# Performance work log

Hardware: AMD Instinct MI355X
Metric: run time of the kernel (lower is better)

The kernel has to match this reference:

```python
import jax, jax.numpy as jnp
import numpy as np

B, S, D, H, DK, DV = 2, 2048, 1024, 16, 64, 64


def setup_inputs() -> dict:
    key = jax.random.key(0)
    ks = jax.random.split(key, 12)
    s = 0.02
    return {
        "q": jax.random.normal(ks[0], (B, S, D), jnp.float32),
        "k": jax.random.normal(ks[1], (B, S, D), jnp.float32),
        "v": jax.random.normal(ks[2], (B, S, D), jnp.float32),
        "attn_mask": jax.random.bernoulli(ks[3], 0.1, (B, S, S)),
        "wq": jax.random.normal(ks[4], (D, H * DK), jnp.float32) * s,
        "bq": jnp.zeros((H * DK,), jnp.float32),
        "wk": jax.random.normal(ks[5], (D, H * DK), jnp.float32) * s,
        "bk": jnp.zeros((H * DK,), jnp.float32),
        "wv": jax.random.normal(ks[6], (D, H * DV), jnp.float32) * s,
        "bv": jnp.zeros((H * DV,), jnp.float32),
        "wo": jax.random.normal(ks[7], (H * DV, D), jnp.float32) * s,
        "bo": jnp.zeros((D,), jnp.float32),
        "gamma": jnp.ones((D,), jnp.float32),
        "beta": jnp.zeros((D,), jnp.float32),
    }


def reference(q, k, v, attn_mask, wq, bq, wk, bk, wv, bv, wo, bo, gamma, beta):
    residual = q
    # projections -> [B, H, S, dk/dv]
    qh = (q @ wq + bq).reshape(B, S, H, DK).transpose(0, 2, 1, 3)
    kh = (k @ wk + bk).reshape(B, S, H, DK).transpose(0, 2, 1, 3)
    vh = (v @ wv + bv).reshape(B, S, H, DV).transpose(0, 2, 1, 3)
    scores = jnp.einsum("bhqd,bhkd->bhqk", qh, kh) / np.sqrt(DK).astype(np.float32)
    scores = jnp.where(attn_mask[:, None, :, :], jnp.float32(-1e9), scores)
    attn = jax.nn.softmax(scores, axis=-1)
    context = jnp.einsum("bhqk,bhkd->bhqd", attn, vh)
    context = context.transpose(0, 2, 1, 3).reshape(B, S, H * DV)
    out = context @ wo + bo + residual
    # LayerNorm (eps=1e-5, torch default)
    mu = out.mean(-1, keepdims=True)
    var = out.var(-1, keepdims=True)
    out = (out - mu) * jax.lax.rsqrt(var + 1e-5) * gamma + beta
    return out, attn
```

## Files before the change

### kernel.cpp

```cpp
#include <hip/hip_runtime.h>
#include <hip/hip_bf16.h>

#define BB 2
#define SS 2048
#define DD 1024
#define HH 16
#define DKV 64

typedef __attribute__((ext_vector_type(8))) short short8;
typedef __attribute__((ext_vector_type(4))) short short4_t;
typedef __attribute__((ext_vector_type(4))) float f32x4;

#define MFMA16(a, b, c) __builtin_amdgcn_mfma_f32_16x16x32_bf16(a, b, c, 0, 0, 0)

__device__ __forceinline__ short f2bf(float f) {
    __hip_bfloat16 h = __float2bfloat16(f);
    union { __hip_bfloat16 h; short s; } u;
    u.h = h;
    return u.s;
}

__global__ __launch_bounds__(256) void wtrans_kernel(
    const float* __restrict__ w0, const float* __restrict__ w1,
    const float* __restrict__ w2, const float* __restrict__ w3,
    const float* __restrict__ qf, const float* __restrict__ kf, const float* __restrict__ vf,
    short* __restrict__ o0, short* __restrict__ o1,
    short* __restrict__ o2, short* __restrict__ o3,
    short* __restrict__ oq, short* __restrict__ ok, short* __restrict__ ov)
{
    const int z = blockIdx.z;
    const int t = threadIdx.x;
    if (z >= 4) {
        const float* src = (z == 4) ? qf : (z == 5) ? kf : vf;
        short* dst = (z == 4) ? oq : (z == 5) ? ok : ov;
        size_t idx = ((size_t)(blockIdx.y * 16 + blockIdx.x) * 256 + t) * 8;
        #pragma unroll
        for (int it = 0; it < 8; ++it, idx += 524288) {
            float4 a = *(const float4*)(src + idx);
            float4 b = *(const float4*)(src + idx + 4);
            short8 p = { f2bf(a.x), f2bf(a.y), f2bf(a.z), f2bf(a.w),
                         f2bf(b.x), f2bf(b.y), f2bf(b.z), f2bf(b.w) };
            *(short8*)(dst + idx) = p;
        }
        return;
    }
    const float* W = (z == 0) ? w0 : (z == 1) ? w1 : (z == 2) ? w2 : w3;
    short* O = (z == 0) ? o0 : (z == 1) ? o1 : (z == 2) ? o2 : o3;
    __shared__ short T[64][72];
    const int k0 = blockIdx.x * 64, n0 = blockIdx.y * 64;
    const int row = t >> 2, c = (t & 3) * 16;
    const float* src = W + (size_t)(k0 + row) * DD + n0 + c;
    #pragma unroll
    for (int i = 0; i < 16; i += 4) {
        float4 f = *(const float4*)(src + i);
        T[c + i + 0][row] = f2bf(f.x);
        T[c + i + 1][row] = f2bf(f.y);
        T[c + i + 2][row] = f2bf(f.z);
        T[c + i + 3][row] = f2bf(f.w);
    }
    __syncthreads();
    const int nr = t >> 2, kc = (t & 3) * 16;
    *(short8*)(O + (size_t)(n0 + nr) * DD + k0 + kc)     = *(const short8*)&T[nr][kc];
    *(short8*)(O + (size_t)(n0 + nr) * DD + k0 + kc + 8) = *(const short8*)&T[nr][kc + 8];
}

__global__ __launch_bounds__(256) void proj3_kernel(
    const short* __restrict__ A0, const short* __restrict__ A1, const short* __restrict__ A2,
    const short* __restrict__ WT0, const short* __restrict__ WT1, const short* __restrict__ WT2,
    const float* __restrict__ bq, const float* __restrict__ bk, const float* __restrict__ bv,
    __hip_bfloat16* __restrict__ o0, __hip_bfloat16* __restrict__ o1, __hip_bfloat16* __restrict__ o2,
    const int* __restrict__ mask, unsigned long long* __restrict__ bits)
{
    const int t = threadIdx.x;
    const int lane = t & 63;
    const int wave = t >> 6;

    if (blockIdx.z == 0) {
        const int bid = blockIdx.y * 32 + blockIdx.x;
        const int base = bid * 512 + wave * 128;
        #pragma unroll 4
        for (int wi = base; wi < base + 128; ++wi) {
            const int mv = mask[(size_t)wi * 64 + lane];
            const unsigned long long bal = __ballot(mv != 0);
            if (lane == 0) bits[wi] = bal;
        }
        return;
    }

    const int z = blockIdx.z - 1;
    const short* A  = (z == 0) ? A0 : (z == 1) ? A1 : A2;
    const short* WT = (z == 0) ? WT0 : (z == 1) ? WT1 : WT2;
    const float* bias = (z == 0) ? bq : (z == 1) ? bk : bv;
    __hip_bfloat16* outh = (z == 0) ? o0 : (z == 1) ? o1 : o2;

    __shared__ __align__(16) short As[128][40];
    __shared__ __align__(16) short Bs[128][40];
    const int wm = wave >> 1, wn = wave & 1;
    const int m0 = blockIdx.x * 128, n0 = blockIdx.y * 128;
    const int lr = lane & 15;
    const int kb = (lane >> 4) * 8;
    const int row2 = t >> 1, kk2 = (t & 1) * 16;

    f32x4 acc[4][4] = {};

    for (int k0 = 0; k0 < DD; k0 += 32) {
        __syncthreads();
        {
            const short8* srca = (const short8*)(A + (size_t)(m0 + row2) * DD + k0 + kk2);
            *(short8*)&As[row2][kk2]     = srca[0];
            *(short8*)&As[row2][kk2 + 8] = srca[1];
        }
        {
            const short8* srcw = (const short8*)(WT + (size_t)(n0 + row2) * DD + k0 + kk2);
            *(short8*)&Bs[row2][kk2]     = srcw[0];
            *(short8*)&Bs[row2][kk2 + 8] = srcw[1];
        }
        __syncthreads();
        short8 af[4], bfr[4];
        #pragma unroll
        for (int i = 0; i < 4; i++) af[i]  = *(const short8*)&As[wm * 64 + i * 16 + lr][kb];
        #pragma unroll
        for (int j = 0; j < 4; j++) bfr[j] = *(const short8*)&Bs[wn * 64 + j * 16 + lr][kb];
        #pragma unroll
        for (int i = 0; i < 4; i++)
            #pragma unroll
            for (int j = 0; j < 4; j++)
                acc[i][j] = MFMA16(af[i], bfr[j], acc[i][j]);
    }

    if (z != 2) {
        #pragma unroll
        for (int j = 0; j < 4; j++) {
            const int col = n0 + wn * 64 + j * 16 + lr;
            const float bvv = bias[col];
            const int h = col >> 6, d = col & 63;
            #pragma unroll
            for (int i = 0; i < 4; i++) {
                #pragma unroll
                for (int r = 0; r < 4; r++) {
                    const int m = m0 + wm * 64 + i * 16 + (lane >> 4) * 4 + r;
                    const int b = m >> 11, s = m & (SS - 1);
                    outh[(((size_t)(b * HH + h)) * SS + s) * DKV + d] =
                        __float2bfloat16(acc[i][j][r] + bvv);
                }
            }
        }
    } else {
        short* vT = (short*)outh;
        #pragma unroll
        for (int j = 0; j < 4; j++) {
            const int col = n0 + wn * 64 + j * 16 + lr;
            const float bvv = bias[col];
            const int h = col >> 6, d = col & 63;
            #pragma unroll
            for (int i = 0; i < 4; i++) {
                const int m = m0 + wm * 64 + i * 16 + (lane >> 4) * 4;
                const int b = m >> 11, s = m & (SS - 1);
                short4_t pk;
                #pragma unroll
                for (int r = 0; r < 4; r++) pk[r] = f2bf(acc[i][j][r] + bvv);
                *(short4_t*)(vT + ((size_t)(b * HH + h) * DKV + d) * SS + s) = pk;
            }
        }
    }
}

__global__ __launch_bounds__(512) void attn_compute_kernel(
    const __hip_bfloat16* __restrict__ qh, const __hip_bfloat16* __restrict__ kh,
    const __hip_bfloat16* __restrict__ vT, const unsigned long long* __restrict__ bits,
    float* __restrict__ linvb, __hip_bfloat16* __restrict__ ctx)
{
    __shared__ __align__(16) short Ks[2][64][72];
    __shared__ __align__(16) short Vs[2][64][72];
    __shared__ __align__(16) short Ps[8][16][72];
    const int t = threadIdx.x, lane = t & 63, w = t >> 6;

    const int logical = (blockIdx.x & 7) * 64 + (blockIdx.x >> 3);
    const int qt = logical & 15;
    const int bh = logical >> 4;
    const int h = bh & (HH - 1);
    const int b = bh >> 4;
    const int q0w = qt * 128 + w * 16;
    const size_t headbase = (size_t)bh * SS * DKV;
    const int lr = lane & 15;
    const int kb = (lane >> 4) * 8;
    const int Q4 = lane >> 4;
    const int rbase = Q4 * 4;

    const short* kbase = (const short*)kh + headbase;
    const short* vbase = (const short*)vT + (size_t)bh * DKV * SS;
    const unsigned long long* bitrow = bits + ((size_t)b * SS + q0w) * (SS / 64);

    const int srow = t >> 3, sc8 = (t & 7) * 8;
    const short* kstg = kbase + (size_t)srow * DKV + sc8;
    const short* vstg = vbase + (size_t)srow * SS + sc8;

    const short* qrp = (const short*)qh + headbase + (size_t)(q0w + lr) * DKV;
    const short8 aq0 = *(const short8*)(qrp + kb);
    const short8 aq1 = *(const short8*)(qrp + 32 + kb);

    float lsum[4] = {0.f, 0.f, 0.f, 0.f};
    f32x4 cacc[4] = {};

    {
        short8 kreg = *(const short8*)(kstg);
        short8 vreg = *(const short8*)(vstg);
        *(short8*)&Ks[0][srow][sc8] = kreg;
        *(short8*)&Vs[0][srow][sc8] = vreg;
        __syncthreads();
        for (int kt = 0; kt < 32; ++kt) {
            const int cur = kt & 1;
            if (kt + 1 < 32) {
                kreg = *(const short8*)(kstg + (size_t)(kt + 1) * 64 * DKV);
                vreg = *(const short8*)(vstg + (size_t)(kt + 1) * 64);
            }
            f32x4 sc[4];
            __builtin_amdgcn_s_setprio(1);
            #pragma unroll
            for (int fc = 0; fc < 4; ++fc) {
                short8 bk0 = *(const short8*)&Ks[cur][fc * 16 + lr][kb];
                short8 bk1 = *(const short8*)&Ks[cur][fc * 16 + lr][32 + kb];
                f32x4 s = {0.f, 0.f, 0.f, 0.f};
                s = MFMA16(aq0, bk0, s);
                s = MFMA16(aq1, bk1, s);
                sc[fc] = s;
            }
            __builtin_amdgcn_s_setprio(0);
            unsigned long long mw[4];
            #pragma unroll
            for (int r = 0; r < 4; ++r)
                mw[r] = bitrow[(size_t)(rbase + r) * (SS / 64) + kt];
            #pragma unroll
            for (int fc = 0; fc < 4; ++fc)
                #pragma unroll
                for (int r = 0; r < 4; ++r) {
                    const bool masked = (mw[r] >> (fc * 16 + lr)) & 1ull;
                    const float p = masked ? 0.f : __expf(sc[fc][r] * 0.125f);
                    lsum[r] += p;
                    Ps[w][rbase + r][fc * 16 + lr] = f2bf(p);
                }
            short8 ap0 = *(const short8*)&Ps[w][lr][kb];
            short8 ap1 = *(const short8*)&Ps[w][lr][32 + kb];
            __builtin_amdgcn_s_setprio(1);
            #pragma unroll
            for (int fd = 0; fd < 4; ++fd) {
                short8 bv0 = *(const short8*)&Vs[cur][fd * 16 + lr][kb];
                short8 bv1 = *(const short8*)&Vs[cur][fd * 16 + lr][32 + kb];
                cacc[fd] = MFMA16(ap0, bv0, cacc[fd]);
                cacc[fd] = MFMA16(ap1, bv1, cacc[fd]);
            }
            __builtin_amdgcn_s_setprio(0);
            if (kt + 1 < 32) {
                *(short8*)&Ks[cur ^ 1][srow][sc8] = kreg;
                *(short8*)&Vs[cur ^ 1][srow][sc8] = vreg;
            }
            __syncthreads();
        }
    }
    #pragma unroll
    for (int r = 0; r < 4; r++) {
        float s = lsum[r];
        s += __shfl_xor(s, 1);
        s += __shfl_xor(s, 2);
        s += __shfl_xor(s, 4);
        s += __shfl_xor(s, 8);
        lsum[r] = s;
    }
    float linv[4];
    #pragma unroll
    for (int r = 0; r < 4; r++) linv[r] = 1.f / lsum[r];

    if (lr == 0) {
        #pragma unroll
        for (int r = 0; r < 4; r++)
            linvb[(size_t)bh * SS + q0w + rbase + r] = linv[r];
    }

    #pragma unroll
    for (int fd = 0; fd < 4; ++fd)
        #pragma unroll
        for (int r = 0; r < 4; r++) {
            const int qrow = q0w + rbase + r;
            ctx[((size_t)b * SS + qrow) * DD + h * DKV + fd * 16 + lr] =
                __float2bfloat16(cacc[fd][r] * linv[r]);
        }
}

__global__ __launch_bounds__(256) void outstore_kernel(
    const __hip_bfloat16* __restrict__ Actx, const short* __restrict__ WT,
    const float* __restrict__ bias, const float* __restrict__ resid,
    float* __restrict__ out,
    const __hip_bfloat16* __restrict__ qh, const __hip_bfloat16* __restrict__ kh,
    const unsigned long long* __restrict__ bits, const float* __restrict__ linvb,
    float* __restrict__ attn)
{
    __shared__ __align__(16) short LDSBUF[36864];
    const int t = threadIdx.x, lane = t & 63, w = t >> 6;
    const int lr = lane & 15;
    const int kb = (lane >> 4) * 8;

    if (blockIdx.z == 0) {
        short (*As)[40] = (short(*)[40])LDSBUF;
        short (*Bs)[40] = (short(*)[40])(LDSBUF + 5120);
        const int wave = w;
        const int wm = wave >> 1, wn = wave & 1;
        const int m0 = blockIdx.x * 128, n0 = blockIdx.y * 128;
        const int row2 = t >> 1, kk2 = (t & 1) * 16;

        f32x4 acc[4][4] = {};

        for (int k0 = 0; k0 < DD; k0 += 32) {
            __syncthreads();
            {
                const short8* src = (const short8*)((const short*)Actx + (size_t)(m0 + row2) * DD + k0 + kk2);
                *(short8*)&As[row2][kk2]     = src[0];
                *(short8*)&As[row2][kk2 + 8] = src[1];
            }
            {
                const short8* srcw = (const short8*)(WT + (size_t)(n0 + row2) * DD + k0 + kk2);
                *(short8*)&Bs[row2][kk2]     = srcw[0];
                *(short8*)&Bs[row2][kk2 + 8] = srcw[1];
            }
            __syncthreads();
            short8 af[4], bfr[4];
            #pragma unroll
            for (int i = 0; i < 4; i++) af[i]  = *(const short8*)&As[wm * 64 + i * 16 + lr][kb];
            #pragma unroll
            for (int j = 0; j < 4; j++) bfr[j] = *(const short8*)&Bs[wn * 64 + j * 16 + lr][kb];
            #pragma unroll
            for (int i = 0; i < 4; i++)
                #pragma unroll
                for (int j = 0; j < 4; j++)
                    acc[i][j] = MFMA16(af[i], bfr[j], acc[i][j]);
        }

        #pragma unroll
        for (int j = 0; j < 4; j++) {
            const int col = n0 + wn * 64 + j * 16 + lr;
            const float bvv = bias[col];
            #pragma unroll
            for (int i = 0; i < 4; i++) {
                #pragma unroll
                for (int r = 0; r < 4; r++) {
                    const int m = m0 + wm * 64 + i * 16 + (lane >> 4) * 4 + r;
                    out[(size_t)m * DD + col] = acc[i][j][r] + bvv + resid[(size_t)m * DD + col];
                }
            }
        }
        return;
    }

    short (*Ks)[72] = (short(*)[72])LDSBUF;
    const int sb = (blockIdx.z - 1) * 256 + blockIdx.y * 32 + blockIdx.x;
    const int qt = sb & 31;
    const int kc = (sb >> 5) & 3;
    const int bh = sb >> 7;
    const int b = bh >> 4;
    const int q0w = qt * 64 + w * 16;
    const int k0c = kc * 512;
    const size_t headbase = (size_t)bh * SS * DKV;
    const int Q4 = lane >> 4;
    const int rbase = Q4 * 4;

    {
        const short* kbase = (const short*)kh + headbase + (size_t)k0c * DKV;
        const int c8 = (t & 7) * 8;
        #pragma unroll
        for (int sweep = 0; sweep < 16; ++sweep) {
            const int row = (t >> 3) + sweep * 32;
            *(short8*)&Ks[row][c8] = *(const short8*)(kbase + (size_t)row * DKV + c8);
        }
    }

    const short* qrp = (const short*)qh + headbase + (size_t)(q0w + lr) * DKV;
    const short8 aq0 = *(const short8*)(qrp + kb);
    const short8 aq1 = *(const short8*)(qrp + 32 + kb);

    float linv[4];
    #pragma unroll
    for (int r = 0; r < 4; ++r)
        linv[r] = linvb[(size_t)bh * SS + q0w + rbase + r];

    const unsigned long long* bitrow = bits + ((size_t)b * SS + q0w) * (SS / 64);
    float* arow = attn + ((size_t)bh * SS + q0w) * SS + k0c;

    __syncthreads();

    for (int g = 0; g < 8; ++g) {
        unsigned long long mw[4];
        #pragma unroll
        for (int r = 0; r < 4; ++r)
            mw[r] = bitrow[(size_t)(rbase + r) * (SS / 64) + kc * 8 + g];
        #pragma unroll
        for (int fc = 0; fc < 4; ++fc) {
            const int col = g * 64 + fc * 16;
            short8 bk0 = *(const short8*)&Ks[col + lr][kb];
            short8 bk1 = *(const short8*)&Ks[col + lr][32 + kb];
            f32x4 s = {0.f, 0.f, 0.f, 0.f};
            s = MFMA16(aq0, bk0, s);
            s = MFMA16(aq1, bk1, s);
            #pragma unroll
            for (int r = 0; r < 4; ++r) {
                const bool masked = (mw[r] >> (fc * 16 + lr)) & 1ull;
                const float p = masked ? 0.f : __expf(s[r] * 0.125f) * linv[r];
                arow[(size_t)(rbase + r) * SS + col + lr] = p;
            }
        }
    }
}

__global__ __launch_bounds__(256) void ln_kernel(
    float* __restrict__ io, const float* __restrict__ g, const float* __restrict__ bta)
{
    const int row = blockIdx.x;
    const int t = threadIdx.x;
    float* p = io + (size_t)row * DD;
    float4 x = *(float4*)(p + t * 4);
    float s  = x.x + x.y + x.z + x.w;
    float s2 = x.x * x.x + x.y * x.y + x.z * x.z + x.w * x.w;
    #pragma unroll
    for (int off = 32; off; off >>= 1) {
        s  += __shfl_xor(s, off);
        s2 += __shfl_xor(s2, off);
    }
    __shared__ float as_[4], bs_[4];
    const int w = t >> 6, l = t & 63;
    if (!l) { as_[w] = s; bs_[w] = s2; }
    __syncthreads();
    s  = as_[0] + as_[1] + as_[2] + as_[3];
    s2 = bs_[0] + bs_[1] + bs_[2] + bs_[3];
    const float mu  = s * (1.f / DD);
    const float var = s2 * (1.f / DD) - mu * mu;
    const float rs  = rsqrtf(var + 1e-5f);
    float4 gv = *(const float4*)(g + t * 4);
    float4 bv = *(const float4*)(bta + t * 4);
    float4 o;
    o.x = (x.x - mu) * rs * gv.x + bv.x;
    o.y = (x.y - mu) * rs * gv.y + bv.y;
    o.z = (x.z - mu) * rs * gv.z + bv.z;
    o.w = (x.w - mu) * rs * gv.w + bv.w;
    *(float4*)(p + t * 4) = o;
}

extern "C" void kernel_launch(void* const* d_in, const int* in_sizes, int n_in,
                              void* d_out, int out_size, void* d_ws, size_t ws_size,
                              hipStream_t stream)
{
    (void)in_sizes; (void)n_in; (void)out_size; (void)ws_size;
    const float* q     = (const float*)d_in[0];
    const float* k     = (const float*)d_in[1];
    const float* v     = (const float*)d_in[2];
    const int*   mask  = (const int*)d_in[3];
    const float* wq    = (const float*)d_in[4];
    const float* bq    = (const float*)d_in[5];
    const float* wk    = (const float*)d_in[6];
    const float* bk    = (const float*)d_in[7];
    const float* wv    = (const float*)d_in[8];
    const float* bv    = (const float*)d_in[9];
    const float* wo    = (const float*)d_in[10];
    const float* bo    = (const float*)d_in[11];
    const float* gamma = (const float*)d_in[12];
    const float* beta  = (const float*)d_in[13];

    float* out  = (float*)d_out;
    float* attn = out + (size_t)BB * SS * DD;

    const size_t hsz = (size_t)BB * HH * SS * DKV;
    __hip_bfloat16* qhp = (__hip_bfloat16*)d_ws;
    __hip_bfloat16* khp = qhp + hsz;
    __hip_bfloat16* vTp = khp + hsz;
    __hip_bfloat16* ctx = vTp + hsz;
    unsigned long long* bits = (unsigned long long*)(ctx + hsz);
    float* linvb = (float*)(bits + (size_t)BB * SS * (SS / 64));
    short* wtq = (short*)(linvb + (size_t)BB * HH * SS);
    short* wtk = wtq + (size_t)DD * DD;
    short* wtv = wtk + (size_t)DD * DD;
    short* wto = wtv + (size_t)DD * DD;
    short* qb  = wto + (size_t)DD * DD;
    short* kb2 = qb  + (size_t)BB * SS * DD;
    short* vb2 = kb2 + (size_t)BB * SS * DD;

    dim3 gw(16, 16, 7);
    wtrans_kernel<<<gw, 256, 0, stream>>>(wq, wk, wv, wo, q, k, v,
                                          wtq, wtk, wtv, wto, qb, kb2, vb2);

    dim3 gg(32, 8, 4);
    proj3_kernel<<<gg, 256, 0, stream>>>(qb, kb2, vb2, wtq, wtk, wtv, bq, bk, bv,
                                         qhp, khp, vTp, mask, bits);
    attn_compute_kernel<<<BB * HH * 16, 512, 0, stream>>>(qhp, khp, vTp, bits, linvb, ctx);

    dim3 gm(32, 8, 17);
    outstore_kernel<<<gm, 256, 0, stream>>>(ctx, wto, bo, q, out,
                                            qhp, khp, bits, linvb, attn);
    ln_kernel<<<BB * SS, 256, 0, stream>>>(out, gamma, beta);
}
```

Before: 330.3 us.

## Split pipeline per batch into uber-kernels overlapping attention with projections and stores

Restructures the launch sequence so each stage runs per batch. Batch-1 projections and mask packing now share a launch with batch-0 attention, and batch-1 attention shares one with batch-0 output projection and attn store. Attention blocks shrink to 256 threads covering 64 query rows, with wider K/V staging per thread. The goal is to fill idle CUs during low-occupancy phases and hide kernel boundaries. In exchange, the uber-kernels have larger unified LDS footprints that may limit occupancy, and block scheduling order decides how much overlap actually happens.

```diff
diff --git a/kernel.cpp b/kernel.cpp
--- a/kernel.cpp
+++ b/kernel.cpp
@@ -20,97 +20,41 @@
     return u.s;
 }
 
-__global__ __launch_bounds__(256) void wtrans_kernel(
-    const float* __restrict__ w0, const float* __restrict__ w1,
-    const float* __restrict__ w2, const float* __restrict__ w3,
-    const float* __restrict__ qf, const float* __restrict__ kf, const float* __restrict__ vf,
-    short* __restrict__ o0, short* __restrict__ o1,
-    short* __restrict__ o2, short* __restrict__ o3,
-    short* __restrict__ oq, short* __restrict__ ok, short* __restrict__ ov)
-{
-    const int z = blockIdx.z;
-    const int t = threadIdx.x;
-    if (z >= 4) {
-        const float* src = (z == 4) ? qf : (z == 5) ? kf : vf;
-        short* dst = (z == 4) ? oq : (z == 5) ? ok : ov;
-        size_t idx = ((size_t)(blockIdx.y * 16 + blockIdx.x) * 256 + t) * 8;
-        #pragma unroll
-        for (int it = 0; it < 8; ++it, idx += 524288) {
-            float4 a = *(const float4*)(src + idx);
-            float4 b = *(const float4*)(src + idx + 4);
-            short8 p = { f2bf(a.x), f2bf(a.y), f2bf(a.z), f2bf(a.w),
-                         f2bf(b.x), f2bf(b.y), f2bf(b.z), f2bf(b.w) };
-            *(short8*)(dst + idx) = p;
-        }
-        return;
-    }
-    const float* W = (z == 0) ? w0 : (z == 1) ? w1 : (z == 2) ? w2 : w3;
-    short* O = (z == 0) ? o0 : (z == 1) ? o1 : (z == 2) ? o2 : o3;
-    __shared__ short T[64][72];
-    const int k0 = blockIdx.x * 64, n0 = blockIdx.y * 64;
-    const int row = t >> 2, c = (t & 3) * 16;
-    const float* src = W + (size_t)(k0 + row) * DD + n0 + c;
-    #pragma unroll
-    for (int i = 0; i < 16; i += 4) {
-        float4 f = *(const float4*)(src + i);
-        T[c + i + 0][row] = f2bf(f.x);
-        T[c + i + 1][row] = f2bf(f.y);
-        T[c + i + 2][row] = f2bf(f.z);
-        T[c + i + 3][row] = f2bf(f.w);
-    }
-    __syncthreads();
-    const int nr = t >> 2, kc = (t & 3) * 16;
-    *(short8*)(O + (size_t)(n0 + nr) * DD + k0 + kc)     = *(const short8*)&T[nr][kc];
-    *(short8*)(O + (size_t)(n0 + nr) * DD + k0 + kc + 8) = *(const short8*)&T[nr][kc + 8];
-}
-
-__global__ __launch_bounds__(256) void proj3_kernel(
-    const short* __restrict__ A0, const short* __restrict__ A1, const short* __restrict__ A2,
-    const short* __restrict__ WT0, const short* __restrict__ WT1, const short* __restrict__ WT2,
-    const float* __restrict__ bq, const float* __restrict__ bk, const float* __restrict__ bv,
-    __hip_bfloat16* __restrict__ o0, __hip_bfloat16* __restrict__ o1, __hip_bfloat16* __restrict__ o2,
-    const int* __restrict__ mask, unsigned long long* __restrict__ bits)
-{
-    const int t = threadIdx.x;
-    const int lane = t & 63;
-    const int wave = t >> 6;
-
-    if (blockIdx.z == 0) {
-        const int bid = blockIdx.y * 32 + blockIdx.x;
-        const int base = bid * 512 + wave * 128;
-        #pragma unroll 4
-        for (int wi = base; wi < base + 128; ++wi) {
-            const int mv = mask[(size_t)wi * 64 + lane];
-            const unsigned long long bal = __ballot(mv != 0);
-            if (lane == 0) bits[wi] = bal;
-        }
-        return;
-    }
-
-    const int z = blockIdx.z - 1;
-    const short* A  = (z == 0) ? A0 : (z == 1) ? A1 : A2;
-    const short* WT = (z == 0) ? WT0 : (z == 1) ? WT1 : WT2;
-    const float* bias = (z == 0) ? bq : (z == 1) ? bk : bv;
-    __hip_bfloat16* outh = (z == 0) ? o0 : (z == 1) ? o1 : o2;
-
-    __shared__ __align__(16) short As[128][40];
-    __shared__ __align__(16) short Bs[128][40];
+
+__device__ __forceinline__ void body_maskpack(
+    const int* __restrict__ mask, unsigned long long* __restrict__ bits,
+    int batch, int bid128)
+{
+    const int t = threadIdx.x, lane = t & 63, wave = t >> 6;
+    const int base = batch * 65536 + bid128 * 512 + wave * 128;
+    #pragma unroll 4
+    for (int wi = base; wi < base + 128; ++wi) {
+        const int mv = mask[(size_t)wi * 64 + lane];
+        const unsigned long long bal = __ballot(mv != 0);
+        if (lane == 0) bits[wi] = bal;
+    }
+}
+
+__device__ __forceinline__ void body_projgemm(
+    const short* __restrict__ A, const short* __restrict__ WT,
+    const float* __restrict__ bias, short* __restrict__ outp,
+    int zmode, int batch, int bx, int by, short* lds)
+{
+    short (*As)[40] = (short(*)[40])lds;
+    short (*Bs)[40] = (short(*)[40])(lds + 5120);
+    const int t = threadIdx.x, lane = t & 63, wave = t >> 6;
     const int wm = wave >> 1, wn = wave & 1;
-    const int m0 = blockIdx.x * 128, n0 = blockIdx.y * 128;
-    const int lr = lane & 15;
-    const int kb = (lane >> 4) * 8;
+    const int m0 = batch * SS + bx * 128, n0 = by * 128;
+    const int lr = lane & 15, kb = (lane >> 4) * 8;
     const int row2 = t >> 1, kk2 = (t & 1) * 16;
 
     f32x4 acc[4][4] = {};
-
     for (int k0 = 0; k0 < DD; k0 += 32) {
         __syncthreads();
         {
             const short8* srca = (const short8*)(A + (size_t)(m0 + row2) * DD + k0 + kk2);
             *(short8*)&As[row2][kk2]     = srca[0];
             *(short8*)&As[row2][kk2 + 8] = srca[1];
-        }
-        {
             const short8* srcw = (const short8*)(WT + (size_t)(n0 + row2) * DD + k0 + kk2);
             *(short8*)&Bs[row2][kk2]     = srcw[0];
             *(short8*)&Bs[row2][kk2 + 8] = srcw[1];
@@ -128,7 +72,7 @@
                 acc[i][j] = MFMA16(af[i], bfr[j], acc[i][j]);
     }
 
-    if (z != 2) {
+    if (zmode != 2) {
         #pragma unroll
         for (int j = 0; j < 4; j++) {
             const int col = n0 + wn * 64 + j * 16 + lr;
@@ -140,13 +84,12 @@
                 for (int r = 0; r < 4; r++) {
                     const int m = m0 + wm * 64 + i * 16 + (lane >> 4) * 4 + r;
                     const int b = m >> 11, s = m & (SS - 1);
-                    outh[(((size_t)(b * HH + h)) * SS + s) * DKV + d] =
-                        __float2bfloat16(acc[i][j][r] + bvv);
+                    outp[(((size_t)(b * HH + h)) * SS + s) * DKV + d] =
+                        f2bf(acc[i][j][r] + bvv);
                 }
             }
         }
     } else {
-        short* vT = (short*)outh;
         #pragma unroll
         for (int j = 0; j < 4; j++) {
             const int col = n0 + wn * 64 + j * 16 + lr;
@@ -159,103 +102,107 @@
                 short4_t pk;
                 #pragma unroll
                 for (int r = 0; r < 4; r++) pk[r] = f2bf(acc[i][j][r] + bvv);
-                *(short4_t*)(vT + ((size_t)(b * HH + h) * DKV + d) * SS + s) = pk;
+                *(short4_t*)(outp + ((size_t)(b * HH + h) * DKV + d) * SS + s) = pk;
             }
         }
     }
 }
 
-__global__ __launch_bounds__(512) void attn_compute_kernel(
-    const __hip_bfloat16* __restrict__ qh, const __hip_bfloat16* __restrict__ kh,
-    const __hip_bfloat16* __restrict__ vT, const unsigned long long* __restrict__ bits,
-    float* __restrict__ linvb, __hip_bfloat16* __restrict__ ctx)
-{
-    __shared__ __align__(16) short Ks[2][64][72];
-    __shared__ __align__(16) short Vs[2][64][72];
-    __shared__ __align__(16) short Ps[8][16][72];
+__device__ __forceinline__ void body_attn(
+    const short* __restrict__ qh, const short* __restrict__ kh,
+    const short* __restrict__ vT, const unsigned long long* __restrict__ bits,
+    float* __restrict__ linvb, short* __restrict__ ctx,
+    int batch, int logical, short* lds)
+{
+    short (*Ks)[64][72] = (short(*)[64][72])lds;
+    short (*Vs)[64][72] = (short(*)[64][72])(lds + 9216);
+    short (*Ps)[16][72] = (short(*)[16][72])(lds + 18432);
     const int t = threadIdx.x, lane = t & 63, w = t >> 6;
-
-    const int logical = (blockIdx.x & 7) * 64 + (blockIdx.x >> 3);
-    const int qt = logical & 15;
-    const int bh = logical >> 4;
-    const int h = bh & (HH - 1);
-    const int b = bh >> 4;
-    const int q0w = qt * 128 + w * 16;
+    const int qt = logical & 31;
+    const int h  = logical >> 5;
+    const int bh = batch * HH + h;
+    const int q0w = qt * 64 + w * 16;
     const size_t headbase = (size_t)bh * SS * DKV;
-    const int lr = lane & 15;
-    const int kb = (lane >> 4) * 8;
-    const int Q4 = lane >> 4;
-    const int rbase = Q4 * 4;
-
-    const short* kbase = (const short*)kh + headbase;
-    const short* vbase = (const short*)vT + (size_t)bh * DKV * SS;
-    const unsigned long long* bitrow = bits + ((size_t)b * SS + q0w) * (SS / 64);
-
-    const int srow = t >> 3, sc8 = (t & 7) * 8;
+    const int lr = lane & 15, kb = (lane >> 4) * 8;
+    const int rbase = (lane >> 4) * 4;
+
+    const short* kbase = kh + headbase;
+    const short* vbase = vT + (size_t)bh * DKV * SS;
+    const unsigned long long* bitrow = bits + ((size_t)batch * SS + q0w) * (SS / 64);
+
+    const int srow = t >> 2, sc8 = (t & 3) * 16;
     const short* kstg = kbase + (size_t)srow * DKV + sc8;
     const short* vstg = vbase + (size_t)srow * SS + sc8;
 
-    const short* qrp = (const short*)qh + headbase + (size_t)(q0w + lr) * DKV;
+    const short* qrp = qh + headbase + (size_t)(q0w + lr) * DKV;
     const short8 aq0 = *(const short8*)(qrp + kb);
     const short8 aq1 = *(const short8*)(qrp + 32 + kb);
 
     float lsum[4] = {0.f, 0.f, 0.f, 0.f};
     f32x4 cacc[4] = {};
 
-    {
-        short8 kreg = *(const short8*)(kstg);
-        short8 vreg = *(const short8*)(vstg);
-        *(short8*)&Ks[0][srow][sc8] = kreg;
-        *(short8*)&Vs[0][srow][sc8] = vreg;
+    short8 ka = *(const short8*)(kstg);
+    short8 kc = *(const short8*)(kstg + 8);
+    short8 va = *(const short8*)(vstg);
+    short8 vc = *(const short8*)(vstg + 8);
+    *(short8*)&Ks[0][srow][sc8]     = ka;
+    *(short8*)&Ks[0][srow][sc8 + 8] = kc;
+    *(short8*)&Vs[0][srow][sc8]     = va;
+    *(short8*)&Vs[0][srow][sc8 + 8] = vc;
+    __syncthreads();
+    for (int kt = 0; kt < 32; ++kt) {
+        const int cur = kt & 1;
+        if (kt + 1 < 32) {
+            const short* kn = kstg + (size_t)(kt + 1) * 64 * DKV;
+            const short* vn = vstg + (size_t)(kt + 1) * 64;
+            ka = *(const short8*)(kn);
+            kc = *(const short8*)(kn + 8);
+            va = *(const short8*)(vn);
+            vc = *(const short8*)(vn + 8);
+        }
+        f32x4 sc[4];
+        __builtin_amdgcn_s_setprio(1);
+        #pragma unroll
+        for (int fc = 0; fc < 4; ++fc) {
+            short8 bk0 = *(const short8*)&Ks[cur][fc * 16 + lr][kb];
+            short8 bk1 = *(const short8*)&Ks[cur][fc * 16 + lr][32 + kb];
+            f32x4 s = {0.f, 0.f, 0.f, 0.f};
+            s = MFMA16(aq0, bk0, s);
+            s = MFMA16(aq1, bk1, s);
+            sc[fc] = s;
+        }
+        __builtin_amdgcn_s_setprio(0);
+        unsigned long long mw[4];
+        #pragma unroll
+        for (int r = 0; r < 4; ++r)
+            mw[r] = bitrow[(size_t)(rbase + r) * (SS / 64) + kt];
+        #pragma unroll
+        for (int fc = 0; fc < 4; ++fc)
+            #pragma unroll
+            for (int r = 0; r < 4; ++r) {
+                const bool masked = (mw[r] >> (fc * 16 + lr)) & 1ull;
+                const float p = masked ? 0.f : __expf(sc[fc][r] * 0.125f);
+                lsum[r] += p;
+                Ps[w][rbase + r][fc * 16 + lr] = f2bf(p);
+            }
+        short8 ap0 = *(const short8*)&Ps[w][lr][kb];
+        short8 ap1 = *(const short8*)&Ps[w][lr][32 + kb];
+        __builtin_amdgcn_s_setprio(1);
+        #pragma unroll
+        for (int fd = 0; fd < 4; ++fd) {
+            short8 bv0 = *(const short8*)&Vs[cur][fd * 16 + lr][kb];
+            short8 bv1 = *(const short8*)&Vs[cur][fd * 16 + lr][32 + kb];
+            cacc[fd] = MFMA16(ap0, bv0, cacc[fd]);
+            cacc[fd] = MFMA16(ap1, bv1, cacc[fd]);
+        }
+        __builtin_amdgcn_s_setprio(0);
+        if (kt + 1 < 32) {
+            *(short8*)&Ks[cur ^ 1][srow][sc8]     = ka;
+            *(short8*)&Ks[cur ^ 1][srow][sc8 + 8] = kc;
+            *(short8*)&Vs[cur ^ 1][srow][sc8]     = va;
+            *(short8*)&Vs[cur ^ 1][srow][sc8 + 8] = vc;
+        }
         __syncthreads();
-        for (int kt = 0; kt < 32; ++kt) {
-            const int cur = kt & 1;
-            if (kt + 1 < 32) {
-                kreg = *(const short8*)(kstg + (size_t)(kt + 1) * 64 * DKV);
-                vreg = *(const short8*)(vstg + (size_t)(kt + 1) * 64);
-            }
-            f32x4 sc[4];
-            __builtin_amdgcn_s_setprio(1);
-            #pragma unroll
-            for (int fc = 0; fc < 4; ++fc) {
-                short8 bk0 = *(const short8*)&Ks[cur][fc * 16 + lr][kb];
-                short8 bk1 = *(const short8*)&Ks[cur][fc * 16 + lr][32 + kb];
-                f32x4 s = {0.f, 0.f, 0.f, 0.f};
-                s = MFMA16(aq0, bk0, s);
-                s = MFMA16(aq1, bk1, s);
-                sc[fc] = s;
-            }
-            __builtin_amdgcn_s_setprio(0);
-            unsigned long long mw[4];
-            #pragma unroll
-            for (int r = 0; r < 4; ++r)
-                mw[r] = bitrow[(size_t)(rbase + r) * (SS / 64) + kt];
-            #pragma unroll
-            for (int fc = 0; fc < 4; ++fc)
-                #pragma unroll
-                for (int r = 0; r < 4; ++r) {
-                    const bool masked = (mw[r] >> (fc * 16 + lr)) & 1ull;
-                    const float p = masked ? 0.f : __expf(sc[fc][r] * 0.125f);
-                    lsum[r] += p;
-                    Ps[w][rbase + r][fc * 16 + lr] = f2bf(p);
-                }
-            short8 ap0 = *(const short8*)&Ps[w][lr][kb];
-            short8 ap1 = *(const short8*)&Ps[w][lr][32 + kb];
-            __builtin_amdgcn_s_setprio(1);
-            #pragma unroll
-            for (int fd = 0; fd < 4; ++fd) {
-                short8 bv0 = *(const short8*)&Vs[cur][fd * 16 + lr][kb];
-                short8 bv1 = *(const short8*)&Vs[cur][fd * 16 + lr][32 + kb];
-                cacc[fd] = MFMA16(ap0, bv0, cacc[fd]);
-                cacc[fd] = MFMA16(ap1, bv1, cacc[fd]);
-            }
-            __builtin_amdgcn_s_setprio(0);
-            if (kt + 1 < 32) {
-                *(short8*)&Ks[cur ^ 1][srow][sc8] = kreg;
-                *(short8*)&Vs[cur ^ 1][srow][sc8] = vreg;
-            }
-            __syncthreads();
-        }
     }
     #pragma unroll
     for (int r = 0; r < 4; r++) {
@@ -275,104 +222,95 @@
         for (int r = 0; r < 4; r++)
             linvb[(size_t)bh * SS + q0w + rbase + r] = linv[r];
     }
-
     #pragma unroll
     for (int fd = 0; fd < 4; ++fd)
         #pragma unroll
         for (int r = 0; r < 4; r++) {
             const int qrow = q0w + rbase + r;
-            ctx[((size_t)b * SS + qrow) * DD + h * DKV + fd * 16 + lr] =
-                __float2bfloat16(cacc[fd][r] * linv[r]);
-        }
-}
-
-__global__ __launch_bounds__(256) void outstore_kernel(
-    const __hip_bfloat16* __restrict__ Actx, const short* __restrict__ WT,
+            ctx[((size_t)batch * SS + qrow) * DD + h * DKV + fd * 16 + lr] =
+                f2bf(cacc[fd][r] * linv[r]);
+        }
+}
+
+__device__ __forceinline__ void body_outproj(
+    const short* __restrict__ Actx, const short* __restrict__ WT,
     const float* __restrict__ bias, const float* __restrict__ resid,
-    float* __restrict__ out,
-    const __hip_bfloat16* __restrict__ qh, const __hip_bfloat16* __restrict__ kh,
+    float* __restrict__ out, int batch, int bx, int by, short* lds)
+{
+    short (*As)[40] = (short(*)[40])lds;
+    short (*Bs)[40] = (short(*)[40])(lds + 5120);
+    const int t = threadIdx.x, lane = t & 63, wave = t >> 6;
+    const int wm = wave >> 1, wn = wave & 1;
+    const int m0 = batch * SS + bx * 128, n0 = by * 128;
+    const int lr = lane & 15, kb = (lane >> 4) * 8;
+    const int row2 = t >> 1, kk2 = (t & 1) * 16;
+
+    f32x4 acc[4][4] = {};
+    for (int k0 = 0; k0 < DD; k0 += 32) {
+        __syncthreads();
+        {
+            const short8* srca = (const short8*)(Actx + (size_t)(m0 + row2) * DD + k0 + kk2);
+            *(short8*)&As[row2][kk2]     = srca[0];
+            *(short8*)&As[row2][kk2 + 8] = srca[1];
+            const short8* srcw = (const short8*)(WT + (size_t)(n0 + row2) * DD + k0 + kk2);
+            *(short8*)&Bs[row2][kk2]     = srcw[0];
+            *(short8*)&Bs[row2][kk2 + 8] = srcw[1];
+        }
+        __syncthreads();
+        short8 af[4], bfr[4];
+        #pragma unroll
+        for (int i = 0; i < 4; i++) af[i]  = *(const short8*)&As[wm * 64 + i * 16 + lr][kb];
+        #pragma unroll
+        for (int j = 0; j < 4; j++) bfr[j] = *(const short8*)&Bs[wn * 64 + j * 16 + lr][kb];
+        #pragma unroll
+        for (int i = 0; i < 4; i++)
+            #pragma unroll
+            for (int j = 0; j < 4; j++)
+                acc[i][j] = MFMA16(af[i], bfr[j], acc[i][j]);
+    }
+    #pragma unroll
+    for (int j = 0; j < 4; j++) {
+        const int col = n0 + wn * 64 + j * 16 + lr;
+        const float bvv = bias[col];
+        #pragma unroll
+        for (int i = 0; i < 4; i++) {
+            #pragma unroll
+            for (int r = 0; r < 4; r++) {
+                const int m = m0 + wm * 64 + i * 16 + (lane >> 4) * 4 + r;
+                out[(size_t)m * DD + col] = acc[i][j][r] + bvv + resid[(size_t)m * DD + col];
+            }
+        }
+    }
+}
+
+__device__ __forceinline__ void body_store(
+    const short* __restrict__ qh, const short* __restrict__ kh,
     const unsigned long long* __restrict__ bits, const float* __restrict__ linvb,
-    float* __restrict__ attn)
-{
-    __shared__ __align__(16) short LDSBUF[36864];
+    float* __restrict__ attn, int batch, int sb, short* lds)
+{
+    short (*Ks)[72] = (short(*)[72])lds;
     const int t = threadIdx.x, lane = t & 63, w = t >> 6;
-    const int lr = lane & 15;
-    const int kb = (lane >> 4) * 8;
-
-    if (blockIdx.z == 0) {
-        short (*As)[40] = (short(*)[40])LDSBUF;
-        short (*Bs)[40] = (short(*)[40])(LDSBUF + 5120);
-        const int wave = w;
-        const int wm = wave >> 1, wn = wave & 1;
-        const int m0 = blockIdx.x * 128, n0 = blockIdx.y * 128;
-        const int row2 = t >> 1, kk2 = (t & 1) * 16;
-
-        f32x4 acc[4][4] = {};
-
-        for (int k0 = 0; k0 < DD; k0 += 32) {
-            __syncthreads();
-            {
-                const short8* src = (const short8*)((const short*)Actx + (size_t)(m0 + row2) * DD + k0 + kk2);
-                *(short8*)&As[row2][kk2]     = src[0];
-                *(short8*)&As[row2][kk2 + 8] = src[1];
-            }
-            {
-                const short8* srcw = (const short8*)(WT + (size_t)(n0 + row2) * DD + k0 + kk2);
-                *(short8*)&Bs[row2][kk2]     = srcw[0];
-                *(short8*)&Bs[row2][kk2 + 8] = srcw[1];
-            }
-            __syncthreads();
-            short8 af[4], bfr[4];
-            #pragma unroll
-            for (int i = 0; i < 4; i++) af[i]  = *(const short8*)&As[wm * 64 + i * 16 + lr][kb];
-            #pragma unroll
-            for (int j = 0; j < 4; j++) bfr[j] = *(const short8*)&Bs[wn * 64 + j * 16 + lr][kb];
-            #pragma unroll
-            for (int i = 0; i < 4; i++)
-                #pragma unroll
-                for (int j = 0; j < 4; j++)
-                    acc[i][j] = MFMA16(af[i], bfr[j], acc[i][j]);
-        }
-
-        #pragma unroll
-        for (int j = 0; j < 4; j++) {
-            const int col = n0 + wn * 64 + j * 16 + lr;
-            const float bvv = bias[col];
-            #pragma unroll
-            for (int i = 0; i < 4; i++) {
-                #pragma unroll
-                for (int r = 0; r < 4; r++) {
-                    const int m = m0 + wm * 64 + i * 16 + (lane >> 4) * 4 + r;
-                    out[(size_t)m * DD + col] = acc[i][j][r] + bvv + resid[(size_t)m * DD + col];
-                }
-            }
-        }
-        return;
-    }
-
-    short (*Ks)[72] = (short(*)[72])LDSBUF;
-    const int sb = (blockIdx.z - 1) * 256 + blockIdx.y * 32 + blockIdx.x;
     const int qt = sb & 31;
     const int kc = (sb >> 5) & 3;
-    const int bh = sb >> 7;
-    const int b = bh >> 4;
+    const int hh = sb >> 7;
+    const int bh = batch * HH + hh;
     const int q0w = qt * 64 + w * 16;
     const int k0c = kc * 512;
     const size_t headbase = (size_t)bh * SS * DKV;
-    const int Q4 = lane >> 4;
-    const int rbase = Q4 * 4;
+    const int lr = lane & 15, kb = (lane >> 4) * 8;
+    const int rbase = (lane >> 4) * 4;
 
     {
-        const short* kbase = (const short*)kh + headbase + (size_t)k0c * DKV;
+        const short* kb2 = kh + headbase + (size_t)k0c * DKV;
         const int c8 = (t & 7) * 8;
         #pragma unroll
         for (int sweep = 0; sweep < 16; ++sweep) {
             const int row = (t >> 3) + sweep * 32;
-            *(short8*)&Ks[row][c8] = *(const short8*)(kbase + (size_t)row * DKV + c8);
-        }
-    }
-
-    const short* qrp = (const short*)qh + headbase + (size_t)(q0w + lr) * DKV;
+            *(short8*)&Ks[row][c8] = *(const short8*)(kb2 + (size_t)row * DKV + c8);
+        }
+    }
+
+    const short* qrp = qh + headbase + (size_t)(q0w + lr) * DKV;
     const short8 aq0 = *(const short8*)(qrp + kb);
     const short8 aq1 = *(const short8*)(qrp + 32 + kb);
 
@@ -381,7 +319,7 @@
     for (int r = 0; r < 4; ++r)
         linv[r] = linvb[(size_t)bh * SS + q0w + rbase + r];
 
-    const unsigned long long* bitrow = bits + ((size_t)b * SS + q0w) * (SS / 64);
+    const unsigned long long* bitrow = bits + ((size_t)batch * SS + q0w) * (SS / 64);
     float* arow = attn + ((size_t)bh * SS + q0w) * SS + k0c;
 
     __syncthreads();
@@ -409,10 +347,10 @@
     }
 }
 
-__global__ __launch_bounds__(256) void ln_kernel(
-    float* __restrict__ io, const float* __restrict__ g, const float* __restrict__ bta)
-{
-    const int row = blockIdx.x;
+__device__ __forceinline__ void body_ln(
+    float* __restrict__ io, const float* __restrict__ g, const float* __restrict__ bta,
+    int row, float* sh)
+{
     const int t = threadIdx.x;
     float* p = io + (size_t)row * DD;
     float4 x = *(float4*)(p + t * 4);
@@ -423,12 +361,11 @@
         s  += __shfl_xor(s, off);
         s2 += __shfl_xor(s2, off);
     }
-    __shared__ float as_[4], bs_[4];
     const int w = t >> 6, l = t & 63;
-    if (!l) { as_[w] = s; bs_[w] = s2; }
+    if (!l) { sh[w] = s; sh[4 + w] = s2; }
     __syncthreads();
-    s  = as_[0] + as_[1] + as_[2] + as_[3];
-    s2 = bs_[0] + bs_[1] + bs_[2] + bs_[3];
+    s  = sh[0] + sh[1] + sh[2] + sh[3];
+    s2 = sh[4] + sh[5] + sh[6] + sh[7];
     const float mu  = s * (1.f / DD);
     const float var = s2 * (1.f / DD) - mu * mu;
     const float rs  = rsqrtf(var + 1e-5f);
@@ -440,6 +377,150 @@
     o.z = (x.z - mu) * rs * gv.z + bv.z;
     o.w = (x.w - mu) * rs * gv.w + bv.w;
     *(float4*)(p + t * 4) = o;
+}
+
+
+__global__ __launch_bounds__(256) void wtrans_kernel(
+    const float* __restrict__ w0, const float* __restrict__ w1,
+    const float* __restrict__ w2, const float* __restrict__ w3,
+    const float* __restrict__ qf, const float* __restrict__ kf, const float* __restrict__ vf,
+    short* __restrict__ o0, short* __restrict__ o1,
+    short* __restrict__ o2, short* __restrict__ o3,
+    short* __restrict__ oq, short* __restrict__ ok, short* __restrict__ ov)
+{
+    const int z = blockIdx.z;
+    const int t = threadIdx.x;
+    if (z >= 4) {
+        const float* src = (z == 4) ? qf : (z == 5) ? kf : vf;
+        short* dst = (z == 4) ? oq : (z == 5) ? ok : ov;
+        size_t idx = ((size_t)(blockIdx.y * 16 + blockIdx.x) * 256 + t) * 8;
+        #pragma unroll
+        for (int it = 0; it < 8; ++it, idx += 524288) {
+            float4 a = *(const float4*)(src + idx);
+            float4 b = *(const float4*)(src + idx + 4);
+            short8 p = { f2bf(a.x), f2bf(a.y), f2bf(a.z), f2bf(a.w),
+                         f2bf(b.x), f2bf(b.y), f2bf(b.z), f2bf(b.w) };
+            *(short8*)(dst + idx) = p;
+        }
+        return;
+    }
+    const float* W = (z == 0) ? w0 : (z == 1) ? w1 : (z == 2) ? w2 : w3;
+    short* O = (z == 0) ? o0 : (z == 1) ? o1 : (z == 2) ? o2 : o3;
+    __shared__ short T[64][72];
+    const int k0 = blockIdx.x * 64, n0 = blockIdx.y * 64;
+    const int row = t >> 2, c = (t & 3) * 16;
+    const float* src = W + (size_t)(k0 + row) * DD + n0 + c;
+    #pragma unroll
+    for (int i = 0; i < 16; i += 4) {
+        float4 f = *(const float4*)(src + i);
+        T[c + i + 0][row] = f2bf(f.x);
+        T[c + i + 1][row] = f2bf(f.y);
+        T[c + i + 2][row] = f2bf(f.z);
+        T[c + i + 3][row] = f2bf(f.w);
+    }
+    __syncthreads();
+    const int nr = t >> 2, kc = (t & 3) * 16;
+    *(short8*)(O + (size_t)(n0 + nr) * DD + k0 + kc)     = *(const short8*)&T[nr][kc];
+    *(short8*)(O + (size_t)(n0 + nr) * DD + k0 + kc + 8) = *(const short8*)&T[nr][kc + 8];
+}
+
+__global__ __launch_bounds__(256) void proj3b_kernel(
+    const short* __restrict__ A0, const short* __restrict__ A1, const short* __restrict__ A2,
+    const short* __restrict__ WT0, const short* __restrict__ WT1, const short* __restrict__ WT2,
+    const float* __restrict__ bq, const float* __restrict__ bk, const float* __restrict__ bv,
+    short* __restrict__ o0, short* __restrict__ o1, short* __restrict__ o2,
+    const int* __restrict__ mask, unsigned long long* __restrict__ bits, int batch)
+{
+    __shared__ __align__(16) short UB[10240];
+    if (blockIdx.z == 0) {
+        body_maskpack(mask, bits, batch, blockIdx.y * 16 + blockIdx.x);
+        return;
+    }
+    const int z = blockIdx.z - 1;
+    const short* A  = (z == 0) ? A0 : (z == 1) ? A1 : A2;
+    const short* WT = (z == 0) ? WT0 : (z == 1) ? WT1 : WT2;
+    const float* bias = (z == 0) ? bq : (z == 1) ? bk : bv;
+    short* outp = (z == 0) ? o0 : (z == 1) ? o1 : o2;
+    body_projgemm(A, WT, bias, outp, z, batch, blockIdx.x, blockIdx.y, UB);
+}
+
+__global__ __launch_bounds__(256) void uber0_kernel(
+    const short* __restrict__ qb, const short* __restrict__ kbf, const short* __restrict__ vbf,
+    const short* __restrict__ WT0, const short* __restrict__ WT1, const short* __restrict__ WT2,
+    const float* __restrict__ bq, const float* __restrict__ bk, const float* __restrict__ bv,
+    short* __restrict__ qh, short* __restrict__ kh, short* __restrict__ vT,
+    const int* __restrict__ mask, unsigned long long* __restrict__ bits,
+    float* __restrict__ linvb, short* __restrict__ ctx)
+{
+    __shared__ __align__(16) short UB[23040];
+    const int bid = blockIdx.x;
+    if (bid < 512) {
+        const int logical = (bid & 7) * 64 + (bid >> 3);
+        body_attn(qh, kh, vT, bits, linvb, ctx, 0, logical, UB);
+        return;
+    }
+    const int rem = bid - 512;
+    if (rem < 384) {
+        const int z = rem >> 7;
+        const int local = rem & 127;
+        const short* A  = (z == 0) ? qb : (z == 1) ? kbf : vbf;
+        const short* WT = (z == 0) ? WT0 : (z == 1) ? WT1 : WT2;
+        const float* bias = (z == 0) ? bq : (z == 1) ? bk : bv;
+        short* outp = (z == 0) ? qh : (z == 1) ? kh : vT;
+        body_projgemm(A, WT, bias, outp, z, 1, local & 15, local >> 4, UB);
+        return;
+    }
+    body_maskpack(mask, bits, 1, rem - 384);
+}
+
+__global__ __launch_bounds__(256) void uber1_kernel(
+    const short* __restrict__ qh, const short* __restrict__ kh, const short* __restrict__ vT,
+    const unsigned long long* __restrict__ bits, float* __restrict__ linvb,
+    short* __restrict__ ctx, const short* __restrict__ WTo,
+    const float* __restrict__ bo, const float* __restrict__ resid,
+    float* __restrict__ out, float* __restrict__ attn)
+{
+    __shared__ __align__(16) short UB[36864];
+    const int bid = blockIdx.x;
+    if (bid < 512) {
+        const int logical = (bid & 7) * 64 + (bid >> 3);
+        body_attn(qh, kh, vT, bits, linvb, ctx, 1, logical, UB);
+        return;
+    }
+    const int rem = bid - 512;
+    if (rem < 128) {
+        body_outproj(ctx, WTo, bo, resid, out, 0, rem & 15, rem >> 4, UB);
+        return;
+    }
+    body_store(qh, kh, bits, linvb, attn, 0, rem - 128, UB);
+}
+
+__global__ __launch_bounds__(256) void uber2_kernel(
+    const short* __restrict__ qh, const short* __restrict__ kh,
+    const unsigned long long* __restrict__ bits, const float* __restrict__ linvb,
+    const short* __restrict__ ctx, const short* __restrict__ WTo,
+    const float* __restrict__ bo, const float* __restrict__ resid,
+    float* __restrict__ out, float* __restrict__ attn,
+    const float* __restrict__ gamma, const float* __restrict__ beta)
+{
+    __shared__ __align__(16) short UB[36864];
+    const int bid = blockIdx.x;
+    if (bid < 128) {
+        body_outproj(ctx, WTo, bo, resid, out, 1, bid & 15, bid >> 4, UB);
+        return;
+    }
+    if (bid < 2176) {
+        body_store(qh, kh, bits, linvb, attn, 1, bid - 128, UB);
+        return;
+    }
+    body_ln(out, gamma, beta, bid - 2176, (float*)UB);
+}
+
+__global__ __launch_bounds__(256) void lnb_kernel(
+    float* __restrict__ io, const float* __restrict__ g, const float* __restrict__ bta)
+{
+    __shared__ float sh[8];
+    body_ln(io, g, bta, SS + blockIdx.x, sh);
 }
 
 extern "C" void kernel_launch(void* const* d_in, const int* in_sizes, int n_in,
@@ -466,10 +547,10 @@
     float* attn = out + (size_t)BB * SS * DD;
 
     const size_t hsz = (size_t)BB * HH * SS * DKV;
-    __hip_bfloat16* qhp = (__hip_bfloat16*)d_ws;
-    __hip_bfloat16* khp = qhp + hsz;
-    __hip_bfloat16* vTp = khp + hsz;
-    __hip_bfloat16* ctx = vTp + hsz;
+    short* qhp = (short*)d_ws;
+    short* khp = qhp + hsz;
+    short* vTp = khp + hsz;
+    short* ctx = vTp + hsz;
     unsigned long long* bits = (unsigned long long*)(ctx + hsz);
     float* linvb = (float*)(bits + (size_t)BB * SS * (SS / 64));
     short* wtq = (short*)(linvb + (size_t)BB * HH * SS);
@@ -484,13 +565,18 @@
     wtrans_kernel<<<gw, 256, 0, stream>>>(wq, wk, wv, wo, q, k, v,
                                           wtq, wtk, wtv, wto, qb, kb2, vb2);
 
-    dim3 gg(32, 8, 4);
-    proj3_kernel<<<gg, 256, 0, stream>>>(qb, kb2, vb2, wtq, wtk, wtv, bq, bk, bv,
-                                         qhp, khp, vTp, mask, bits);
-    attn_compute_kernel<<<BB * HH * 16, 512, 0, stream>>>(qhp, khp, vTp, bits, linvb, ctx);
-
-    dim3 gm(32, 8, 17);
-    outstore_kernel<<<gm, 256, 0, stream>>>(ctx, wto, bo, q, out,
-                                            qhp, khp, bits, linvb, attn);
-    ln_kernel<<<BB * SS, 256, 0, stream>>>(out, gamma, beta);
-}
+    dim3 gg(16, 8, 4);
+    proj3b_kernel<<<gg, 256, 0, stream>>>(qb, kb2, vb2, wtq, wtk, wtv, bq, bk, bv,
+                                          qhp, khp, vTp, mask, bits, 0);
+
+    uber0_kernel<<<1024, 256, 0, stream>>>(qb, kb2, vb2, wtq, wtk, wtv, bq, bk, bv,
+                                           qhp, khp, vTp, mask, bits, linvb, ctx);
+
+    uber1_kernel<<<2688, 256, 0, stream>>>(qhp, khp, vTp, bits, linvb, ctx,
+                                           wto, bo, q, out, attn);
+
+    uber2_kernel<<<4224, 256, 0, stream>>>(qhp, khp, bits, linvb, ctx,
+                                           wto, bo, q, out, attn, gamma, beta);
+
+    lnb_kernel<<<SS, 256, 0, stream>>>(out, gamma, beta);
+}
```

New measurement: 403.4 us. 1.22x slower.
